# Performance work log

Hardware: AMD Instinct MI355X
Metric: run time of the kernel (lower is better)

Reference implementation:

```python
import jax, jax.numpy as jnp
import numpy as np

B, T, N, D, H = 16, 16, 184, 128, 8
HD = D // H  # 16
EMB = 10


def _forward(dim, query, key, value, Wq, bq, Wk, bk, Wv, bv, Wm, bm, Wo, bo, ne1, ne2):
    B0 = query.shape[0]
    D0 = Wq.shape[0]
    HD0 = Wm.shape[0]
    H0 = D0 // HD0
    q = query @ Wq.T + bq
    k = key @ Wk.T + bk
    v = value @ Wv.T + bv

    def split_heads(x):  # [B, A, C, D] -> [H*B, A, C, HD], head-major (torch split+cat)
        x = x.reshape(x.shape[:-1] + (H0, HD0))
        x = jnp.moveaxis(x, -2, 0)  # [H, B, A, C, HD]
        return x.reshape((H0 * B0,) + x.shape[2:])

    q, k, v = split_heads(q), split_heads(k), split_heads(v)
    # attention over the last spatial axis: scores [H*B, T, N, N]
    attn = jnp.matmul(q, jnp.swapaxes(k, -1, -2)) / jnp.sqrt(jnp.asarray(HD0, q.dtype))
    attn_row = jax.nn.softmax(attn, axis=-1)
    attn_col = jax.nn.softmax(attn, axis=-2)
    o1 = jnp.matmul(attn_row, v)
    o2 = jnp.matmul(jnp.swapaxes(attn_col, -1, -2), v)
    adp = ne1 @ ne2  # [184, 184]
    adp_row = jax.nn.softmax(adp, axis=-1)
    adp_col = jax.nn.softmax(adp, axis=0)
    if dim == 2:
        o3 = jnp.einsum('ik,btkf->btif', adp_row, v)
        o4 = jnp.einsum('ik,btkf->btif', adp_col.T, v)
        out = jnp.concatenate([o1, o2, o3, o4], axis=-1)  # [H*B, T, N, 4*HD]
        out = out @ Wm.T + bm  # [H*B, T, N, HD]
    else:  # dim == 1
        o3 = jnp.einsum('ik,bktf->bitf', adp_row, v)
        o4 = jnp.einsum('ik,bktf->bitf', adp_col.T, v)
        cat = jnp.concatenate([o1, o2, o3, o4], axis=-1)
        filt = cat @ Wm.T + bm
        gate = jnp.tanh(cat[..., :HD0]) * jax.nn.sigmoid(cat[..., -HD0:])
        out = filt + gate
    # merge heads back: [H*B, ..., HD] -> [B, ..., H*HD]
    out = out.reshape((H0, B0) + out.shape[1:])
    out = jnp.moveaxis(out, 0, -2)
    out = out.reshape(out.shape[:-2] + (H0 * HD0,))
    return out @ Wo.T + bo


def setup_inputs() -> dict:
    rng = jax.random.key(0)
    ks = jax.random.split(rng, 16)
    n = lambda i, shape, s=1.0: jax.random.normal(ks[i], shape, dtype=jnp.float32) * s
    return {
        'query': n(0, (B, T, N, D)),
        'key': n(1, (B, T, N, D)),
        'value': n(2, (B, T, N, D)),
        'Wq': n(3, (D, D), 0.05), 'bq': n(4, (D,), 0.05),
        'Wk': n(5, (D, D), 0.05), 'bk': n(6, (D,), 0.05),
        'Wv': n(7, (D, D), 0.05), 'bv': n(8, (D,), 0.05),
        'Wm': n(9, (HD, 4 * HD), 0.05), 'bm': n(10, (HD,), 0.05),
        'Wo': n(11, (D, D), 0.05), 'bo': n(12, (D,), 0.05),
        'ne1': n(13, (N, EMB)),
        'ne2': n(14, (EMB, N)),
        'dim': 2,
    }


def reference(query, key, value, Wq, bq, Wk, bk, Wv, bv, Wm, bm, Wo, bo, ne1, ne2, dim):
    return _forward(dim, query, key, value, Wq, bq, Wk, bk, Wv, bv, Wm, bm, Wo, bo, ne1, ne2)
```

## Files before the change

### kernel.cpp

```cpp
#include <hip/hip_runtime.h>

typedef unsigned int u32;
typedef unsigned short u16;
typedef unsigned long long ull;

constexpr int kB = 16, kT = 16, kN = 184, kD = 128, kH = 8, kHD = 16;
constexpr int kBT = kB * kT;
constexpr int kRows = kBT * kN;
constexpr int kTile = kN * kHD;
#define KQSCALE 0.36067376022224085f

typedef __attribute__((ext_vector_type(8))) short bf16x8;
typedef __attribute__((ext_vector_type(4))) float f32x4;

union FragU {
  bf16x8 f;
  ull u[2];
  uint4 q;
  u16 h[8];
};

#define MFMA(a, b, c) __builtin_amdgcn_mfma_f32_16x16x32_bf16((a), (b), (c), 0, 0, 0)

__device__ __forceinline__ float bf2f(u16 v) {
  return __uint_as_float(((u32)v) << 16);
}
__device__ __forceinline__ u16 f2bf(float f) {
  u32 x = __float_as_uint(f);
  x += 0x7fffu + ((x >> 16) & 1u);
  return (u16)(x >> 16);
}
__device__ __forceinline__ u32 pack_bf2(float lo, float hi) {
  u32 a = __float_as_uint(lo); a += 0x7fffu + ((a >> 16) & 1u);
  u32 b = __float_as_uint(hi); b += 0x7fffu + ((b >> 16) & 1u);
  return __builtin_amdgcn_perm(b, a, 0x07060302);
}
__device__ __forceinline__ u32 pack_trunc(float lo, float hi) {
  return __builtin_amdgcn_perm(__float_as_uint(hi), __float_as_uint(lo), 0x07060302);
}
__device__ __forceinline__ u16 trunc_bf(float f) {
  return (u16)(__float_as_uint(f) >> 16);
}

__global__ __launch_bounds__(256) void wcvt_kernel(
    const float* __restrict__ Wq, const float* __restrict__ Wk,
    const float* __restrict__ Wv, const float* __restrict__ Wo,
    u16* __restrict__ wb) {
  const int t = blockIdx.x * 256 + threadIdx.x;
  if (t >= 8192) return;
  u32* dst = (u32*)wb;
  float2 a = ((const float2*)Wq)[t]; dst[t]          = pack_bf2(a.x, a.y);
  float2 b = ((const float2*)Wk)[t]; dst[8192 + t]   = pack_bf2(b.x, b.y);
  float2 c = ((const float2*)Wv)[t]; dst[16384 + t]  = pack_bf2(c.x, c.y);
  float2 d = ((const float2*)Wo)[t]; dst[24576 + t]  = pack_bf2(d.x, d.y);
}

__global__ __launch_bounds__(256) void adp_kernel(
    const float* __restrict__ ne1, const float* __restrict__ ne2,
    u16* __restrict__ arr3, u16* __restrict__ arr4) {
  __shared__ float s1[kN * 10];
  __shared__ float s2[10 * kN];
  __shared__ float l1r[kN];
  __shared__ float l2c[kN];
  const int tid = threadIdx.x;
  for (int i = tid; i < kN * 10; i += 256) { s1[i] = ne1[i]; s2[i] = ne2[i]; }
  __syncthreads();

  if (tid < kN) {
    const int r = tid;
    float reg[10];
#pragma unroll
    for (int e = 0; e < 10; ++e) reg[e] = s1[r * 10 + e];
    float sum = 0.f;
    for (int c = 0; c < kN; ++c) {
      float d = 0.f;
#pragma unroll
      for (int e = 0; e < 10; ++e) d += reg[e] * s2[e * kN + c];
      sum += __expf(d);
    }
    l1r[r] = sum;

    const int c = tid;
    float regc[10];
#pragma unroll
    for (int e = 0; e < 10; ++e) regc[e] = s2[e * kN + c];
    sum = 0.f;
    for (int r2 = 0; r2 < kN; ++r2) {
      float d = 0.f;
#pragma unroll
      for (int e = 0; e < 10; ++e) d += s1[r2 * 10 + e] * regc[e];
      sum += __expf(d);
    }
    l2c[c] = sum;
  }
  __syncthreads();

  for (int ee = blockIdx.x * 256 + tid; ee < 12 * 6 * 64; ee += 12 * 256) {
    const int i = ee / 384;
    const int rem = ee - i * 384;
    const int p = rem >> 6;
    const int lane = rem & 63;
    const int row = i * 16 + (lane & 15);
    const int cb = p * 32 + (lane >> 4) * 8;
    FragU fo3, fo4;
    const bool rok = row < kN;
    float inv1 = 0.f, inv2 = 0.f;
    float rreg[10], creg[10];
    if (rok) {
      inv1 = 1.f / l1r[row];
      inv2 = 1.f / l2c[row];
#pragma unroll
      for (int e = 0; e < 10; ++e) {
        rreg[e] = s1[row * 10 + e];
        creg[e] = s2[e * kN + row];
      }
    }
#pragma unroll
    for (int j = 0; j < 8; ++j) {
      const int col = cb + j;
      float v3 = 0.f, v4 = 0.f;
      if (rok && col < kN) {
        float d3 = 0.f, d4 = 0.f;
#pragma unroll
        for (int e = 0; e < 10; ++e) {
          d3 += rreg[e] * s2[e * kN + col];
          d4 += s1[col * 10 + e] * creg[e];
        }
        v3 = __expf(d3) * inv1;
        v4 = __expf(d4) * inv2;
      }
      fo3.h[j] = f2bf(v3);
      fo4.h[j] = f2bf(v4);
    }
    *(uint4*)(arr3 + (size_t)ee * 8) = fo3.q;
    *(uint4*)(arr4 + (size_t)ee * 8) = fo4.q;
  }
}

__global__ __launch_bounds__(256) void proj_kernel(
    const float* __restrict__ qin, const float* __restrict__ kin, const float* __restrict__ vin,
    const u16* __restrict__ wb,
    const float* __restrict__ bq, const float* __restrict__ bk, const float* __restrict__ bv,
    u16* __restrict__ qo, u16* __restrict__ ko, u16* __restrict__ vo) {
  __shared__ u16 s_w[128 * 136];
  __shared__ u16 s_a[128 * 136];

  const float* in; const u16* W; const float* bias; u16* out; float scale;
  if (blockIdx.y == 0)      { in = qin; W = wb;         bias = bq; out = qo; scale = KQSCALE; }
  else if (blockIdx.y == 1) { in = kin; W = wb + 16384; bias = bk; out = ko; scale = 1.f; }
  else                      { in = vin; W = wb + 32768; bias = bv; out = vo; scale = 1.f; }

  const int tid = threadIdx.x;
  const int r0 = blockIdx.x * 128;
  {
    const uint4* src = (const uint4*)W;
    for (int i = tid; i < 2048; i += 256) {
      const int row = i >> 4, q16 = i & 15;
      *(uint4*)(s_w + row * 136 + q16 * 8) = src[i];
    }
    const float* abase = in + (size_t)r0 * 128;
#pragma unroll
    for (int i = 0; i < 16; ++i) {
      const int idx = i * 1024 + tid * 4;
      const float4 v = *(const float4*)(abase + idx);
      const int row = idx >> 7, col = idx & 127;
      *(u32*)(s_a + row * 136 + col)     = pack_bf2(v.x, v.y);
      *(u32*)(s_a + row * 136 + col + 2) = pack_bf2(v.z, v.w);
    }
  }
  __syncthreads();

  const int w = tid >> 6, lane = tid & 63, quad = lane >> 4, m = lane & 15;

  f32x4 acc0[8], acc1[8];
  const f32x4 z4 = {0.f, 0.f, 0.f, 0.f};
#pragma unroll
  for (int ct = 0; ct < 8; ++ct) { acc0[ct] = z4; acc1[ct] = z4; }

  const u16* ap0 = s_a + (w * 16 + m) * 136 + quad * 8;
  const u16* ap1 = ap0 + 64 * 136;

#pragma unroll
  for (int kp = 0; kp < 4; ++kp) {
    FragU a0; a0.q = *(const uint4*)(ap0 + kp * 32);
    FragU a1; a1.q = *(const uint4*)(ap1 + kp * 32);
#pragma unroll
    for (int ct = 0; ct < 8; ++ct) {
      FragU bfr; bfr.q = *(const uint4*)(s_w + (ct * 16 + m) * 136 + kp * 32 + quad * 8);
      acc0[ct] = MFMA(a0.f, bfr.f, acc0[ct]);
      acc1[ct] = MFMA(a1.f, bfr.f, acc1[ct]);
    }
  }

  float bc[8];
#pragma unroll
  for (int ct = 0; ct < 8; ++ct) bc[ct] = bias[ct * 16 + m];

#pragma unroll
  for (int half = 0; half < 2; ++half) {
    const f32x4* acc = half ? acc1 : acc0;
    const int rbase = r0 + (w + half * 4) * 16 + quad * 4;
#pragma unroll
    for (int rr = 0; rr < 4; ++rr) {
      const int r = rbase + rr;
      const int bt = r / kN;
      const int n = r - bt * kN;
      u16* op = out + ((size_t)bt * kN + n) * 16 + m;
#pragma unroll
      for (int ct = 0; ct < 8; ++ct)
        op[(size_t)ct * kBT * kN * 16] = f2bf((acc[ct][rr] + bc[ct]) * scale);
    }
  }
}

__global__ __launch_bounds__(256, 2) void attn_kernel(
    const u16* qg, const u16* __restrict__ kg, const u16* __restrict__ vg,
    const u16* __restrict__ arr3, const u16* __restrict__ arr4,
    const float* __restrict__ Wm, const float* __restrict__ bm,
    u16* mg) {
  __shared__ u16 pool[39424];
  u16* const s_E   = pool;
  u16* const s_ET0 = pool + 13824;
  u16* const s_ET1 = pool + 26624;
  u16* const s_vT  = s_ET1;
  u16* const s_cat = s_ET1;

  const int tid = threadIdx.x;
  const size_t base = (size_t)blockIdx.x * kTile;
  const int w = tid >> 6, lane = tid & 63;
  const int quad = lane >> 4, m = lane & 15;

  for (int idx = tid; idx < 3072; idx += 256) {
    const int t = idx >> 4, ch = idx & 15;
    s_vT[ch * 200 + t] = (t < kN) ? vg[base + idx] : (u16)0;
  }

  bf16x8 kfr[12];
#pragma unroll
  for (int t12 = 0; t12 < 12; ++t12) {
    FragU fk; fk.u[0] = 0; fk.u[1] = 0;
    const int tok = t12 * 16 + m;
    if (quad < 2 && tok < kN)
      fk.q = *(const uint4*)(kg + base + tok * 16 + quad * 8);
    kfr[t12] = fk.f;
  }
  bf16x8 qB[3];
#pragma unroll
  for (int ti = 0; ti < 3; ++ti) {
    FragU fq; fq.u[0] = 0; fq.u[1] = 0;
    const int tok = (w + ti * 4) * 16 + m;
    if (quad < 2 && tok < kN)
      fq.q = *(const uint4*)(qg + base + tok * 16 + quad * 8);
    qB[ti] = fq.f;
  }

  bf16x8 wmb[2];
#pragma unroll
  for (int kt = 0; kt < 2; ++kt) {
    FragU f;
#pragma unroll
    for (int j = 0; j < 8; ++j) {
      const int kdl = quad * 8 + j;
      const int orig = (kt * 2 + (kdl & 1)) * 16 + (kdl >> 1);
      f.h[j] = f2bf(Wm[m * 64 + orig]);
    }
    wmb[kt] = f.f;
  }
  const float4 bm4 = *(const float4*)(bm + quad * 4);

  __syncthreads();

  bf16x8 vb[6];
#pragma unroll
  for (int p = 0; p < 6; ++p) {
    FragU f;
    f.q = *(const uint4*)(s_vT + m * 200 + p * 32 + quad * 8);
    vb[p] = f.f;
  }
  FragU onesU; onesU.u[0] = 0x3F803F803F803F80ULL; onesU.u[1] = onesU.u[0];
  const bf16x8 ones = onesU.f;
  const f32x4 zero4 = {0.f, 0.f, 0.f, 0.f};

  f32x4 o1[3], l1[3], o3[3], o4[3], o2[3], l2[3];
#pragma unroll
  for (int ti = 0; ti < 3; ++ti) {
    o1[ti] = zero4; l1[ti] = zero4; o3[ti] = zero4;
    o4[ti] = zero4; o2[ti] = zero4; l2[ti] = zero4;
  }

#define S_PHASE(CC, ETB)                                                      \
  do {                                                                        \
    _Pragma("unroll") for (int ti = 0; ti < 3; ++ti) {                        \
      const int qt = w + ti * 4;                                              \
      const int qrow = qt * 16 + m;                                           \
      _Pragma("unroll") for (int ktl = 0; ktl < 4; ++ktl) {                   \
        f32x4 sv = MFMA(kfr[(CC) * 4 + ktl], qB[ti], zero4);                  \
        const float e0 = exp2f(sv[0]), e1 = exp2f(sv[1]);                     \
        const float e2 = exp2f(sv[2]), e3 = exp2f(sv[3]);                     \
        uint2 ev;                                                             \
        ev.x = pack_trunc(e0, e1);                                            \
        ev.y = pack_trunc(e2, e3);                                            \
        *(uint2*)(s_E + qrow * 72 + ktl * 16 + quad * 4) = ev;                \
        u16* etp = (ETB) + (ktl * 16 + quad * 4) * 200 + qrow;                \
        etp[0]   = trunc_bf(e0);                                              \
        etp[200] = trunc_bf(e1);                                              \
        etp[400] = trunc_bf(e2);                                              \
        etp[600] = trunc_bf(e3);                                              \
      }                                                                       \
    }                                                                         \
  } while (0)

#define LOAD_ARR(CC)                                                          \
  _Pragma("unroll") for (int ti = 0; ti < 3; ++ti) {                          \
    const int qt = w + ti * 4;                                                \
    _Pragma("unroll") for (int pl = 0; pl < 2; ++pl) {                        \
      const int pg = (CC) * 2 + pl;                                           \
      a3f[ti * 2 + pl].q = *(const uint4*)(arr3 + (size_t)((qt * 6 + pg) * 64 + lane) * 8); \
      a4f[ti * 2 + pl].q = *(const uint4*)(arr4 + (size_t)((qt * 6 + pg) * 64 + lane) * 8); \
    }                                                                         \
  }

#define ROW_PHASE(CC)                                                         \
  _Pragma("unroll") for (int ti = 0; ti < 3; ++ti) {                          \
    const int qt = w + ti * 4;                                                \
    const u16* erp = s_E + (qt * 16 + m) * 72 + quad * 8;                     \
    _Pragma("unroll") for (int pl = 0; pl < 2; ++pl) {                        \
      const int pg = (CC) * 2 + pl;                                           \
      FragU pa; pa.q = *(const uint4*)(erp + pl * 32);                        \
      o1[ti] = MFMA(pa.f, vb[pg], o1[ti]);                                    \
      l1[ti] = MFMA(pa.f, ones, l1[ti]);                                      \
      o3[ti] = MFMA(a3f[ti * 2 + pl].f, vb[pg], o3[ti]);                      \
      o4[ti] = MFMA(a4f[ti * 2 + pl].f, vb[pg], o4[ti]);                      \
    }                                                                         \
  }

#define COL_PHASE(CC, ETB)                                                    \
  {                                                                           \
    const u16* etr = (ETB) + (w * 16 + m) * 200 + quad * 8;                   \
    _Pragma("unroll") for (int pg = 0; pg < 6; ++pg) {                        \
      FragU pT; pT.q = *(const uint4*)(etr + pg * 32);                        \
      o2[CC] = MFMA(pT.f, vb[pg], o2[CC]);                                    \
      l2[CC] = MFMA(pT.f, ones, l2[CC]);                                      \
    }                                                                         \
  }

  S_PHASE(0, s_ET0);
  __syncthreads();
  {
    FragU a3f[6], a4f[6];
    LOAD_ARR(0);
    COL_PHASE(0, s_ET0);
    ROW_PHASE(0);
    S_PHASE(1, s_ET1);
  }
  __syncthreads();
  {
    FragU a3f[6], a4f[6];
    LOAD_ARR(1);
    COL_PHASE(1, s_ET1);
    ROW_PHASE(1);
    S_PHASE(2, s_ET0);
  }
  __syncthreads();
  {
    FragU a3f[6], a4f[6];
    LOAD_ARR(2);
    COL_PHASE(2, s_ET0);
    ROW_PHASE(2);
  }

#undef S_PHASE
#undef LOAD_ARR
#undef ROW_PHASE
#undef COL_PHASE

  u16* cw = s_cat + w * 1152;
#pragma unroll
  for (int ti = 0; ti < 3; ++ti) {
    const int tt = w + ti * 4;
#pragma unroll
    for (int r = 0; r < 4; ++r) {
      const int token = quad * 4 + r;
      const float n1 = o1[ti][r] * __builtin_amdgcn_rcpf(l1[ti][r] - 8.0f);
      const float n2 = o2[ti][r] * __builtin_amdgcn_rcpf(l2[ti][r] - 8.0f);
      *(u32*)(cw + token * 72 + 2 * m)      = pack_bf2(n1, n2);
      *(u32*)(cw + token * 72 + 32 + 2 * m) = pack_bf2(o3[ti][r], o4[ti][r]);
    }
    f32x4 macc = {bm4.x, bm4.y, bm4.z, bm4.w};
#pragma unroll
    for (int kt = 0; kt < 2; ++kt) {
      FragU ca; ca.q = *(const uint4*)(cw + m * 72 + kt * 32 + quad * 8);
      macc = MFMA(wmb[kt], ca.f, macc);
    }
    if (tt * 16 + m < kN) {
      *(uint2*)(mg + base + (tt * 16 + m) * 16 + quad * 4) =
          make_uint2(pack_bf2(macc[0], macc[1]), pack_bf2(macc[2], macc[3]));
    }
  }
}

__global__ __launch_bounds__(256) void out_kernel(
    const u16* __restrict__ mg, const u16* __restrict__ wob,
    const float* __restrict__ bo, float* __restrict__ outg) {
  __shared__ u16 s_w[128 * 136];
  const int tid = threadIdx.x;
  {
    const uint4* src = (const uint4*)wob;
    for (int i = tid; i < 2048; i += 256) {
      const int row = i >> 4, q16 = i & 15;
      *(uint4*)(s_w + row * 136 + q16 * 8) = src[i];
    }
  }
  __syncthreads();

  const int w = tid >> 6, lane = tid & 63, quad = lane >> 4, m = lane & 15;
  const int r0 = blockIdx.x * 128;

  f32x4 acc0[8], acc1[8];
  const f32x4 z4 = {0.f, 0.f, 0.f, 0.f};
#pragma unroll
  for (int ct = 0; ct < 8; ++ct) { acc0[ct] = z4; acc1[ct] = z4; }

  const int hh = quad >> 1, hd8 = (quad & 1) * 8;
  const int ra = r0 + w * 16 + m;
  const int bt0 = ra / kN, n0 = ra - bt0 * kN;
  const int rb = ra + 64;
  const int bt1 = rb / kN, n1 = rb - bt1 * kN;
  const u16* mp0 = mg + ((size_t)(hh * kBT + bt0) * kN + n0) * 16 + hd8;
  const u16* mp1 = mg + ((size_t)(hh * kBT + bt1) * kN + n1) * 16 + hd8;
  const size_t hstep = (size_t)2 * kBT * kN * 16;

#pragma unroll
  for (int kp = 0; kp < 4; ++kp) {
    FragU a0; a0.q = *(const uint4*)(mp0 + kp * hstep);
    FragU a1; a1.q = *(const uint4*)(mp1 + kp * hstep);
#pragma unroll
    for (int ct = 0; ct < 8; ++ct) {
      FragU bfr; bfr.q = *(const uint4*)(s_w + (ct * 16 + m) * 136 + kp * 32 + quad * 8);
      acc0[ct] = MFMA(a0.f, bfr.f, acc0[ct]);
      acc1[ct] = MFMA(a1.f, bfr.f, acc1[ct]);
    }
  }

  float bc[8];
#pragma unroll
  for (int ct = 0; ct < 8; ++ct) bc[ct] = bo[ct * 16 + m];

#pragma unroll
  for (int half = 0; half < 2; ++half) {
    const f32x4* acc = half ? acc1 : acc0;
    const int rbase = r0 + (w + half * 4) * 16 + quad * 4;
#pragma unroll
    for (int rr = 0; rr < 4; ++rr) {
      float* op = outg + (size_t)(rbase + rr) * 128 + m;
#pragma unroll
      for (int ct = 0; ct < 8; ++ct)
        op[ct * 16] = acc[ct][rr] + bc[ct];
    }
  }
}

extern "C" void kernel_launch(void* const* d_in, const int* in_sizes, int n_in,
                              void* d_out, int out_size, void* d_ws, size_t ws_size,
                              hipStream_t stream) {
  const float* query = (const float*)d_in[0];
  const float* key   = (const float*)d_in[1];
  const float* value = (const float*)d_in[2];
  const float* Wq = (const float*)d_in[3];
  const float* bq = (const float*)d_in[4];
  const float* Wk = (const float*)d_in[5];
  const float* bk = (const float*)d_in[6];
  const float* Wv = (const float*)d_in[7];
  const float* bv = (const float*)d_in[8];
  const float* Wm = (const float*)d_in[9];
  const float* bm = (const float*)d_in[10];
  const float* Wo = (const float*)d_in[11];
  const float* bo = (const float*)d_in[12];
  const float* ne1 = (const float*)d_in[13];
  const float* ne2 = (const float*)d_in[14];

  const size_t tensor_bytes = (size_t)kH * kB * kT * kN * kHD * 2;
  const size_t frag_bytes = (size_t)12 * 6 * 64 * 8 * 2;
  char* ws = (char*)d_ws;
  u16* qs   = (u16*)(ws);
  u16* ks   = (u16*)(ws + tensor_bytes);
  u16* vs   = (u16*)(ws + 2 * tensor_bytes);
  u16* arr3 = (u16*)(ws + 3 * tensor_bytes);
  u16* arr4 = (u16*)(ws + 3 * tensor_bytes + frag_bytes);
  u16* wb   = (u16*)(ws + 3 * tensor_bytes + 2 * frag_bytes);

  wcvt_kernel<<<32, 256, 0, stream>>>(Wq, Wk, Wv, Wo, wb);
  adp_kernel<<<12, 256, 0, stream>>>(ne1, ne2, arr3, arr4);
  proj_kernel<<<dim3(kRows / 128, 3), 256, 0, stream>>>(
      query, key, value, wb, bq, bk, bv, qs, ks, vs);
  attn_kernel<<<kH * kB * kT, 256, 0, stream>>>(qs, ks, vs, arr3, arr4, Wm, bm, qs);
  out_kernel<<<kRows / 128, 256, 0, stream>>>(qs, wb + 49152, bo, (float*)d_out);
}
```

Baseline: 241.5 us.

## Shrink attention LDS to single ET buffer for 3 blocks/CU; fuse weight conversion

Restructures the attention kernel so each wave computes scores for its own key tile against all query tiles, which lets the transposed-exp buffer become per-wave. The double-buffered ET region is dropped, cutting shared memory from about 77KB to 52KB, and launch bounds are raised to 3 blocks per CU for more occupancy. In exchange, S-phase no longer overlaps with the previous column/row phase and extra barriers are added. Separately, the weight bf16 conversion is folded into the adp kernel, removing one launch.

```diff
diff --git a/kernel.cpp b/kernel.cpp
--- a/kernel.cpp
+++ b/kernel.cpp
@@ -42,27 +42,28 @@
   return (u16)(__float_as_uint(f) >> 16);
 }
 
-__global__ __launch_bounds__(256) void wcvt_kernel(
+__global__ __launch_bounds__(256) void adp_kernel(
+    const float* __restrict__ ne1, const float* __restrict__ ne2,
+    u16* __restrict__ arr3, u16* __restrict__ arr4,
     const float* __restrict__ Wq, const float* __restrict__ Wk,
     const float* __restrict__ Wv, const float* __restrict__ Wo,
     u16* __restrict__ wb) {
-  const int t = blockIdx.x * 256 + threadIdx.x;
-  if (t >= 8192) return;
-  u32* dst = (u32*)wb;
-  float2 a = ((const float2*)Wq)[t]; dst[t]          = pack_bf2(a.x, a.y);
-  float2 b = ((const float2*)Wk)[t]; dst[8192 + t]   = pack_bf2(b.x, b.y);
-  float2 c = ((const float2*)Wv)[t]; dst[16384 + t]  = pack_bf2(c.x, c.y);
-  float2 d = ((const float2*)Wo)[t]; dst[24576 + t]  = pack_bf2(d.x, d.y);
-}
-
-__global__ __launch_bounds__(256) void adp_kernel(
-    const float* __restrict__ ne1, const float* __restrict__ ne2,
-    u16* __restrict__ arr3, u16* __restrict__ arr4) {
   __shared__ float s1[kN * 10];
   __shared__ float s2[10 * kN];
   __shared__ float l1r[kN];
   __shared__ float l2c[kN];
   const int tid = threadIdx.x;
+
+  {
+    u32* dst = (u32*)wb;
+    for (int t = blockIdx.x * 256 + tid; t < 8192; t += 12 * 256) {
+      float2 a = ((const float2*)Wq)[t]; dst[t]          = pack_bf2(a.x, a.y);
+      float2 b = ((const float2*)Wk)[t]; dst[8192 + t]   = pack_bf2(b.x, b.y);
+      float2 c = ((const float2*)Wv)[t]; dst[16384 + t]  = pack_bf2(c.x, c.y);
+      float2 d = ((const float2*)Wo)[t]; dst[24576 + t]  = pack_bf2(d.x, d.y);
+    }
+  }
+
   for (int i = tid; i < kN * 10; i += 256) { s1[i] = ne1[i]; s2[i] = ne2[i]; }
   __syncthreads();
 
@@ -213,45 +214,44 @@
   }
 }
 
-__global__ __launch_bounds__(256, 2) void attn_kernel(
+__global__ __launch_bounds__(256, 3) void attn_kernel(
     const u16* qg, const u16* __restrict__ kg, const u16* __restrict__ vg,
     const u16* __restrict__ arr3, const u16* __restrict__ arr4,
     const float* __restrict__ Wm, const float* __restrict__ bm,
     u16* mg) {
-  __shared__ u16 pool[39424];
-  u16* const s_E   = pool;
-  u16* const s_ET0 = pool + 13824;
-  u16* const s_ET1 = pool + 26624;
-  u16* const s_vT  = s_ET1;
-  u16* const s_cat = s_ET1;
+  __shared__ u16 pool[26624];
+  u16* const s_E  = pool;
+  u16* const s_ET = pool + 13824;
+  u16* const s_vT = pool;
 
   const int tid = threadIdx.x;
   const size_t base = (size_t)blockIdx.x * kTile;
   const int w = tid >> 6, lane = tid & 63;
   const int quad = lane >> 4, m = lane & 15;
+  u16* const ET_w = s_ET + w * 3200;
 
   for (int idx = tid; idx < 3072; idx += 256) {
     const int t = idx >> 4, ch = idx & 15;
     s_vT[ch * 200 + t] = (t < kN) ? vg[base + idx] : (u16)0;
   }
 
-  bf16x8 kfr[12];
+  bf16x8 kOwn[3];
+#pragma unroll
+  for (int c = 0; c < 3; ++c) {
+    FragU fk; fk.u[0] = 0; fk.u[1] = 0;
+    const int tok = (c * 4 + w) * 16 + m;
+    if (quad < 2 && tok < kN)
+      fk.q = *(const uint4*)(kg + base + tok * 16 + quad * 8);
+    kOwn[c] = fk.f;
+  }
+  bf16x8 qAll[12];
 #pragma unroll
   for (int t12 = 0; t12 < 12; ++t12) {
-    FragU fk; fk.u[0] = 0; fk.u[1] = 0;
+    FragU fq; fq.u[0] = 0; fq.u[1] = 0;
     const int tok = t12 * 16 + m;
     if (quad < 2 && tok < kN)
-      fk.q = *(const uint4*)(kg + base + tok * 16 + quad * 8);
-    kfr[t12] = fk.f;
-  }
-  bf16x8 qB[3];
-#pragma unroll
-  for (int ti = 0; ti < 3; ++ti) {
-    FragU fq; fq.u[0] = 0; fq.u[1] = 0;
-    const int tok = (w + ti * 4) * 16 + m;
-    if (quad < 2 && tok < kN)
       fq.q = *(const uint4*)(qg + base + tok * 16 + quad * 8);
-    qB[ti] = fq.f;
+    qAll[t12] = fq.f;
   }
 
   bf16x8 wmb[2];
@@ -277,6 +277,8 @@
     f.q = *(const uint4*)(s_vT + m * 200 + p * 32 + quad * 8);
     vb[p] = f.f;
   }
+  __syncthreads();
+
   FragU onesU; onesU.u[0] = 0x3F803F803F803F80ULL; onesU.u[1] = onesU.u[0];
   const bf16x8 ones = onesU.f;
   const f32x4 zero4 = {0.f, 0.f, 0.f, 0.f};
@@ -288,25 +290,21 @@
     o4[ti] = zero4; o2[ti] = zero4; l2[ti] = zero4;
   }
 
-#define S_PHASE(CC, ETB)                                                      \
+#define S_PHASE(CC)                                                           \
   do {                                                                        \
-    _Pragma("unroll") for (int ti = 0; ti < 3; ++ti) {                        \
-      const int qt = w + ti * 4;                                              \
-      const int qrow = qt * 16 + m;                                           \
-      _Pragma("unroll") for (int ktl = 0; ktl < 4; ++ktl) {                   \
-        f32x4 sv = MFMA(kfr[(CC) * 4 + ktl], qB[ti], zero4);                  \
-        const float e0 = exp2f(sv[0]), e1 = exp2f(sv[1]);                     \
-        const float e2 = exp2f(sv[2]), e3 = exp2f(sv[3]);                     \
-        uint2 ev;                                                             \
-        ev.x = pack_trunc(e0, e1);                                            \
-        ev.y = pack_trunc(e2, e3);                                            \
-        *(uint2*)(s_E + qrow * 72 + ktl * 16 + quad * 4) = ev;                \
-        u16* etp = (ETB) + (ktl * 16 + quad * 4) * 200 + qrow;                \
-        etp[0]   = trunc_bf(e0);                                              \
-        etp[200] = trunc_bf(e1);                                              \
-        etp[400] = trunc_bf(e2);                                              \
-        etp[600] = trunc_bf(e3);                                              \
-      }                                                                       \
+    _Pragma("unroll") for (int qt = 0; qt < 12; ++qt) {                       \
+      f32x4 sv = MFMA(kOwn[CC], qAll[qt], zero4);                             \
+      const float e0 = exp2f(sv[0]), e1 = exp2f(sv[1]);                       \
+      const float e2 = exp2f(sv[2]), e3 = exp2f(sv[3]);                       \
+      uint2 evv;                                                              \
+      evv.x = pack_trunc(e0, e1);                                             \
+      evv.y = pack_trunc(e2, e3);                                             \
+      *(uint2*)(s_E + (qt * 16 + m) * 72 + w * 16 + quad * 4) = evv;          \
+      u16* etp = ET_w + (quad * 4) * 200 + qt * 16 + m;                       \
+      etp[0]   = trunc_bf(e0);                                                \
+      etp[200] = trunc_bf(e1);                                                \
+      etp[400] = trunc_bf(e2);                                                \
+      etp[600] = trunc_bf(e3);                                                \
     }                                                                         \
   } while (0)
 
@@ -334,9 +332,9 @@
     }                                                                         \
   }
 
-#define COL_PHASE(CC, ETB)                                                    \
+#define COL_PHASE(CC)                                                         \
   {                                                                           \
-    const u16* etr = (ETB) + (w * 16 + m) * 200 + quad * 8;                   \
+    const u16* etr = ET_w + m * 200 + quad * 8;                               \
     _Pragma("unroll") for (int pg = 0; pg < 6; ++pg) {                        \
       FragU pT; pT.q = *(const uint4*)(etr + pg * 32);                        \
       o2[CC] = MFMA(pT.f, vb[pg], o2[CC]);                                    \
@@ -344,28 +342,30 @@
     }                                                                         \
   }
 
-  S_PHASE(0, s_ET0);
+  S_PHASE(0);
   __syncthreads();
   {
     FragU a3f[6], a4f[6];
     LOAD_ARR(0);
-    COL_PHASE(0, s_ET0);
+    COL_PHASE(0);
     ROW_PHASE(0);
-    S_PHASE(1, s_ET1);
-  }
+  }
+  __syncthreads();
+  S_PHASE(1);
   __syncthreads();
   {
     FragU a3f[6], a4f[6];
     LOAD_ARR(1);
-    COL_PHASE(1, s_ET1);
+    COL_PHASE(1);
     ROW_PHASE(1);
-    S_PHASE(2, s_ET0);
-  }
+  }
+  __syncthreads();
+  S_PHASE(2);
   __syncthreads();
   {
     FragU a3f[6], a4f[6];
     LOAD_ARR(2);
-    COL_PHASE(2, s_ET0);
+    COL_PHASE(2);
     ROW_PHASE(2);
   }
 
@@ -374,7 +374,7 @@
 #undef ROW_PHASE
 #undef COL_PHASE
 
-  u16* cw = s_cat + w * 1152;
+  u16* cw = ET_w;
 #pragma unroll
   for (int ti = 0; ti < 3; ++ti) {
     const int tt = w + ti * 4;
@@ -489,8 +489,7 @@
   u16* arr4 = (u16*)(ws + 3 * tensor_bytes + frag_bytes);
   u16* wb   = (u16*)(ws + 3 * tensor_bytes + 2 * frag_bytes);
 
-  wcvt_kernel<<<32, 256, 0, stream>>>(Wq, Wk, Wv, Wo, wb);
-  adp_kernel<<<12, 256, 0, stream>>>(ne1, ne2, arr3, arr4);
+  adp_kernel<<<12, 256, 0, stream>>>(ne1, ne2, arr3, arr4, Wq, Wk, Wv, Wo, wb);
   proj_kernel<<<dim3(kRows / 128, 3), 256, 0, stream>>>(
       query, key, value, wb, bq, bk, bv, qs, ks, vs);
   attn_kernel<<<kH * kB * kT, 256, 0, stream>>>(qs, ks, vs, arr3, arr4, Wm, bm, qs);
```

Result: slower. 274.6 us (+13.7%).

## Fold weight conversion and adjacency softmax into projection kernel launch

Applied to the files above, without the earlier changes.

Removes the separate weight-conversion and adjacency kernels. The projection and output kernels now read fp32 weights and pack them to bf16 while staging them into shared memory. The adjacency softmax work moves into an extra blockIdx.y==3 slice of the projection grid, so it runs alongside the projections. This saves two launches and their serial gaps. In exchange every projection block re-converts its weights from fp32, and the extra grid slice launches many blocks that exit immediately.

```diff
diff --git a/kernel.cpp b/kernel.cpp
--- a/kernel.cpp
+++ b/kernel.cpp
@@ -42,121 +42,115 @@
   return (u16)(__float_as_uint(f) >> 16);
 }
 
-__global__ __launch_bounds__(256) void wcvt_kernel(
-    const float* __restrict__ Wq, const float* __restrict__ Wk,
-    const float* __restrict__ Wv, const float* __restrict__ Wo,
-    u16* __restrict__ wb) {
-  const int t = blockIdx.x * 256 + threadIdx.x;
-  if (t >= 8192) return;
-  u32* dst = (u32*)wb;
-  float2 a = ((const float2*)Wq)[t]; dst[t]          = pack_bf2(a.x, a.y);
-  float2 b = ((const float2*)Wk)[t]; dst[8192 + t]   = pack_bf2(b.x, b.y);
-  float2 c = ((const float2*)Wv)[t]; dst[16384 + t]  = pack_bf2(c.x, c.y);
-  float2 d = ((const float2*)Wo)[t]; dst[24576 + t]  = pack_bf2(d.x, d.y);
-}
-
-__global__ __launch_bounds__(256) void adp_kernel(
+__global__ __launch_bounds__(256) void proj_kernel(
+    const float* __restrict__ qin, const float* __restrict__ kin, const float* __restrict__ vin,
+    const float* __restrict__ Wq, const float* __restrict__ Wk, const float* __restrict__ Wv,
+    const float* __restrict__ bq, const float* __restrict__ bk, const float* __restrict__ bv,
+    u16* __restrict__ qo, u16* __restrict__ ko, u16* __restrict__ vo,
     const float* __restrict__ ne1, const float* __restrict__ ne2,
     u16* __restrict__ arr3, u16* __restrict__ arr4) {
-  __shared__ float s1[kN * 10];
-  __shared__ float s2[10 * kN];
-  __shared__ float l1r[kN];
-  __shared__ float l2c[kN];
+  __shared__ float smem_f[17408];
   const int tid = threadIdx.x;
-  for (int i = tid; i < kN * 10; i += 256) { s1[i] = ne1[i]; s2[i] = ne2[i]; }
-  __syncthreads();
-
-  if (tid < kN) {
-    const int r = tid;
-    float reg[10];
-#pragma unroll
-    for (int e = 0; e < 10; ++e) reg[e] = s1[r * 10 + e];
-    float sum = 0.f;
-    for (int c = 0; c < kN; ++c) {
-      float d = 0.f;
-#pragma unroll
-      for (int e = 0; e < 10; ++e) d += reg[e] * s2[e * kN + c];
-      sum += __expf(d);
-    }
-    l1r[r] = sum;
-
-    const int c = tid;
-    float regc[10];
-#pragma unroll
-    for (int e = 0; e < 10; ++e) regc[e] = s2[e * kN + c];
-    sum = 0.f;
-    for (int r2 = 0; r2 < kN; ++r2) {
-      float d = 0.f;
-#pragma unroll
-      for (int e = 0; e < 10; ++e) d += s1[r2 * 10 + e] * regc[e];
-      sum += __expf(d);
-    }
-    l2c[c] = sum;
-  }
-  __syncthreads();
-
-  for (int ee = blockIdx.x * 256 + tid; ee < 12 * 6 * 64; ee += 12 * 256) {
-    const int i = ee / 384;
-    const int rem = ee - i * 384;
-    const int p = rem >> 6;
-    const int lane = rem & 63;
-    const int row = i * 16 + (lane & 15);
-    const int cb = p * 32 + (lane >> 4) * 8;
-    FragU fo3, fo4;
-    const bool rok = row < kN;
-    float inv1 = 0.f, inv2 = 0.f;
-    float rreg[10], creg[10];
-    if (rok) {
-      inv1 = 1.f / l1r[row];
-      inv2 = 1.f / l2c[row];
-#pragma unroll
-      for (int e = 0; e < 10; ++e) {
-        rreg[e] = s1[row * 10 + e];
-        creg[e] = s2[e * kN + row];
+
+  if (blockIdx.y == 3) {
+    if (blockIdx.x >= 12) return;
+    float* const s1  = smem_f;
+    float* const s2  = smem_f + 1840;
+    float* const l1r = smem_f + 3680;
+    float* const l2c = smem_f + 3864;
+
+    for (int i = tid; i < kN * 10; i += 256) { s1[i] = ne1[i]; s2[i] = ne2[i]; }
+    __syncthreads();
+
+    if (tid < kN) {
+      const int r = tid;
+      float reg[10];
+#pragma unroll
+      for (int e = 0; e < 10; ++e) reg[e] = s1[r * 10 + e];
+      float sum = 0.f;
+      for (int c = 0; c < kN; ++c) {
+        float d = 0.f;
+#pragma unroll
+        for (int e = 0; e < 10; ++e) d += reg[e] * s2[e * kN + c];
+        sum += __expf(d);
       }
-    }
-#pragma unroll
-    for (int j = 0; j < 8; ++j) {
-      const int col = cb + j;
-      float v3 = 0.f, v4 = 0.f;
-      if (rok && col < kN) {
-        float d3 = 0.f, d4 = 0.f;
+      l1r[r] = sum;
+
+      const int c = tid;
+      float regc[10];
+#pragma unroll
+      for (int e = 0; e < 10; ++e) regc[e] = s2[e * kN + c];
+      sum = 0.f;
+      for (int r2 = 0; r2 < kN; ++r2) {
+        float d = 0.f;
+#pragma unroll
+        for (int e = 0; e < 10; ++e) d += s1[r2 * 10 + e] * regc[e];
+        sum += __expf(d);
+      }
+      l2c[c] = sum;
+    }
+    __syncthreads();
+
+    for (int ee = blockIdx.x * 256 + tid; ee < 12 * 6 * 64; ee += 12 * 256) {
+      const int i = ee / 384;
+      const int rem = ee - i * 384;
+      const int p = rem >> 6;
+      const int lane = rem & 63;
+      const int row = i * 16 + (lane & 15);
+      const int cb = p * 32 + (lane >> 4) * 8;
+      FragU fo3, fo4;
+      const bool rok = row < kN;
+      float inv1 = 0.f, inv2 = 0.f;
+      float rreg[10], creg[10];
+      if (rok) {
+        inv1 = 1.f / l1r[row];
+        inv2 = 1.f / l2c[row];
 #pragma unroll
         for (int e = 0; e < 10; ++e) {
-          d3 += rreg[e] * s2[e * kN + col];
-          d4 += s1[col * 10 + e] * creg[e];
+          rreg[e] = s1[row * 10 + e];
+          creg[e] = s2[e * kN + row];
         }
-        v3 = __expf(d3) * inv1;
-        v4 = __expf(d4) * inv2;
       }
-      fo3.h[j] = f2bf(v3);
-      fo4.h[j] = f2bf(v4);
-    }
-    *(uint4*)(arr3 + (size_t)ee * 8) = fo3.q;
-    *(uint4*)(arr4 + (size_t)ee * 8) = fo4.q;
-  }
-}
-
-__global__ __launch_bounds__(256) void proj_kernel(
-    const float* __restrict__ qin, const float* __restrict__ kin, const float* __restrict__ vin,
-    const u16* __restrict__ wb,
-    const float* __restrict__ bq, const float* __restrict__ bk, const float* __restrict__ bv,
-    u16* __restrict__ qo, u16* __restrict__ ko, u16* __restrict__ vo) {
-  __shared__ u16 s_w[128 * 136];
-  __shared__ u16 s_a[128 * 136];
-
-  const float* in; const u16* W; const float* bias; u16* out; float scale;
-  if (blockIdx.y == 0)      { in = qin; W = wb;         bias = bq; out = qo; scale = KQSCALE; }
-  else if (blockIdx.y == 1) { in = kin; W = wb + 16384; bias = bk; out = ko; scale = 1.f; }
-  else                      { in = vin; W = wb + 32768; bias = bv; out = vo; scale = 1.f; }
-
-  const int tid = threadIdx.x;
+#pragma unroll
+      for (int j = 0; j < 8; ++j) {
+        const int col = cb + j;
+        float v3 = 0.f, v4 = 0.f;
+        if (rok && col < kN) {
+          float d3 = 0.f, d4 = 0.f;
+#pragma unroll
+          for (int e = 0; e < 10; ++e) {
+            d3 += rreg[e] * s2[e * kN + col];
+            d4 += s1[col * 10 + e] * creg[e];
+          }
+          v3 = __expf(d3) * inv1;
+          v4 = __expf(d4) * inv2;
+        }
+        fo3.h[j] = f2bf(v3);
+        fo4.h[j] = f2bf(v4);
+      }
+      *(uint4*)(arr3 + (size_t)ee * 8) = fo3.q;
+      *(uint4*)(arr4 + (size_t)ee * 8) = fo4.q;
+    }
+    return;
+  }
+
+  u16* const s_w = (u16*)smem_f;
+  u16* const s_a = (u16*)smem_f + 128 * 136;
+
+  const float* in; const float* Wf; const float* bias; u16* out; float scale;
+  if (blockIdx.y == 0)      { in = qin; Wf = Wq; bias = bq; out = qo; scale = KQSCALE; }
+  else if (blockIdx.y == 1) { in = kin; Wf = Wk; bias = bk; out = ko; scale = 1.f; }
+  else                      { in = vin; Wf = Wv; bias = bv; out = vo; scale = 1.f; }
+
   const int r0 = blockIdx.x * 128;
   {
-    const uint4* src = (const uint4*)W;
     for (int i = tid; i < 2048; i += 256) {
-      const int row = i >> 4, q16 = i & 15;
-      *(uint4*)(s_w + row * 136 + q16 * 8) = src[i];
+      const int row = i >> 4, c8 = (i & 15) * 8;
+      const float4 w0 = *(const float4*)(Wf + row * 128 + c8);
+      const float4 w1 = *(const float4*)(Wf + row * 128 + c8 + 4);
+      *(uint4*)(s_w + row * 136 + c8) =
+          make_uint4(pack_bf2(w0.x, w0.y), pack_bf2(w0.z, w0.w),
+                     pack_bf2(w1.x, w1.y), pack_bf2(w1.z, w1.w));
     }
     const float* abase = in + (size_t)r0 * 128;
 #pragma unroll
@@ -400,15 +394,18 @@
 }
 
 __global__ __launch_bounds__(256) void out_kernel(
-    const u16* __restrict__ mg, const u16* __restrict__ wob,
+    const u16* __restrict__ mg, const float* __restrict__ Wo,
     const float* __restrict__ bo, float* __restrict__ outg) {
   __shared__ u16 s_w[128 * 136];
   const int tid = threadIdx.x;
   {
-    const uint4* src = (const uint4*)wob;
     for (int i = tid; i < 2048; i += 256) {
-      const int row = i >> 4, q16 = i & 15;
-      *(uint4*)(s_w + row * 136 + q16 * 8) = src[i];
+      const int row = i >> 4, c8 = (i & 15) * 8;
+      const float4 w0 = *(const float4*)(Wo + row * 128 + c8);
+      const float4 w1 = *(const float4*)(Wo + row * 128 + c8 + 4);
+      *(uint4*)(s_w + row * 136 + c8) =
+          make_uint4(pack_bf2(w0.x, w0.y), pack_bf2(w0.z, w0.w),
+                     pack_bf2(w1.x, w1.y), pack_bf2(w1.z, w1.w));
     }
   }
   __syncthreads();
@@ -487,12 +484,10 @@
   u16* vs   = (u16*)(ws + 2 * tensor_bytes);
   u16* arr3 = (u16*)(ws + 3 * tensor_bytes);
   u16* arr4 = (u16*)(ws + 3 * tensor_bytes + frag_bytes);
-  u16* wb   = (u16*)(ws + 3 * tensor_bytes + 2 * frag_bytes);
-
-  wcvt_kernel<<<32, 256, 0, stream>>>(Wq, Wk, Wv, Wo, wb);
-  adp_kernel<<<12, 256, 0, stream>>>(ne1, ne2, arr3, arr4);
-  proj_kernel<<<dim3(kRows / 128, 3), 256, 0, stream>>>(
-      query, key, value, wb, bq, bk, bv, qs, ks, vs);
+
+  proj_kernel<<<dim3(kRows / 128, 4), 256, 0, stream>>>(
+      query, key, value, Wq, Wk, Wv, bq, bk, bv, qs, ks, vs,
+      ne1, ne2, arr3, arr4);
   attn_kernel<<<kH * kB * kT, 256, 0, stream>>>(qs, ks, vs, arr3, arr4, Wm, bm, qs);
-  out_kernel<<<kRows / 128, 256, 0, stream>>>(qs, wb + 49152, bo, (float*)d_out);
-}
+  out_kernel<<<kRows / 128, 256, 0, stream>>>(qs, Wo, bo, (float*)d_out);
+}
```

Measured after the change: 230.0 us. -4.8%, faster.
